# Optimization experiments

Hardware: AMD Instinct MI355X
Metric: run time of the kernel (lower is better)

Reference implementation:

```python
import jax, jax.numpy as jnp
import numpy as np

B, H, S, D = 4, 16, 2048, 64
NEG = -1000000000.0


def setup_inputs() -> dict:
    key = jax.random.key(0)
    kq, kk, kv, km = jax.random.split(key, 4)
    Q = jax.random.normal(kq, (B, H, S, D), dtype=jnp.float32)
    K = jax.random.normal(kk, (B, H, S, D), dtype=jnp.float32)
    V = jax.random.normal(kv, (B, H, S, D), dtype=jnp.float32)
    attn_mask = jax.random.randint(km, (B, 1, 1, S), 0, 2).astype(jnp.bool_)
    return {"Q": Q, "K": K, "V": V, "attn_mask": attn_mask}


def reference(Q, K, V, attn_mask):
    scale = 1.0 / (Q.shape[-1] ** 0.5)
    # [B,H,S,S] scores, masked, softmax over keys
    scores = jnp.einsum("bhqd,bhkd->bhqk", Q, K) * scale
    scores = jnp.where(attn_mask, NEG, scores)
    attn_prob = jax.nn.softmax(scores, axis=-1)
    context = jnp.einsum("bhqk,bhkd->bhqd", attn_prob, V)
    return context
```

## Files before the change

### kernel.cpp

```cpp
#include <hip/hip_runtime.h>
#include <hip/hip_bf16.h>

#define B_ 4
#define H_ 16
#define S_ 2048
#define D_ 64
#define BH_ (B_ * H_)
#define VSTR 2048

#define QS 0.18033688011112042f

typedef __bf16 bf16_t;
typedef __attribute__((ext_vector_type(8))) bf16_t bf16x8;
typedef __attribute__((ext_vector_type(4))) bf16_t bf16x4;
typedef __attribute__((ext_vector_type(4))) float f32x4;

#if __has_builtin(__builtin_amdgcn_exp2f)
#define EX2(x) __builtin_amdgcn_exp2f(x)
#else
#define EX2(x) exp2f(x)
#endif

#define KC_OFF 0u
#define VT_OFF 16777216u
#define CIDX_OFF 33554432u
#define NK_OFF 33619968u

__device__ __forceinline__ bf16x4 cvt4(const float4 a) {
  return (bf16x4){(bf16_t)a.x, (bf16_t)a.y, (bf16_t)a.z, (bf16_t)a.w};
}

__global__ __launch_bounds__(256) void scan_kernel(const unsigned char* __restrict__ raw,
                                                   int* __restrict__ cidx,
                                                   int* __restrict__ nkarr) {
  const int b = blockIdx.x;
  const int tid = threadIdx.x;
  __shared__ int isBool;
  if (tid == 0) isBool = 0;
  __syncthreads();
  int any = 0;
  for (int i = tid; i < B_ * S_; i += 256)
    if ((i & 3) && raw[i]) any = 1;
  if (any) isBool = 1;
  __syncthreads();
  const bool ib = (isBool != 0);

  int flags[8], cnt = 0;
  const int base = tid * 8;
#pragma unroll
  for (int j = 0; j < 8; ++j) {
    const int key = base + j;
    const int m = ib ? (raw[b * S_ + key] ? 1 : 0)
                     : (((const int*)raw)[b * S_ + key] ? 1 : 0);
    flags[j] = m ? 0 : 1;
    cnt += flags[j];
  }
  __shared__ int sc[256];
  sc[tid] = cnt;
  __syncthreads();
  for (int off = 1; off < 256; off <<= 1) {
    const int v = sc[tid];
    const int u = (tid >= off) ? sc[tid - off] : 0;
    __syncthreads();
    sc[tid] = v + u;
    __syncthreads();
  }
  int pos = (tid > 0) ? sc[tid - 1] : 0;
  const int total = sc[255];
  int* cb = cidx + b * VSTR;
#pragma unroll
  for (int j = 0; j < 8; ++j)
    if (flags[j]) cb[pos++] = base + j;
  if (tid == 0) nkarr[b] = total;
  const int padend = ((total + 63) >> 6) << 6;
  for (int i = total + tid; i < padend; i += 256) cb[i] = 0;
}

__global__ __launch_bounds__(256) void gather_kernel(const float* __restrict__ K,
                                                     const float* __restrict__ V,
                                                     const int* __restrict__ cidx,
                                                     const int* __restrict__ nkarr,
                                                     bf16_t* __restrict__ Kc,
                                                     bf16_t* __restrict__ Vtc) {
  const int blk = blockIdx.x;
  const int bh = blk >> 5, tile = blk & 31;
  const int b = bh >> 4;
  if (tile * 64 >= nkarr[b]) return;
  const int tid = threadIdx.x;
  __shared__ int idx[64];
  __shared__ float T[64][65];
  if (tid < 64) idx[tid] = cidx[b * VSTR + tile * 64 + tid];
  __syncthreads();
  {
    const int row = tid >> 2, d0 = (tid & 3) << 4;
    const float* src = K + (size_t)bh * S_ * D_ + (size_t)idx[row] * D_ + d0;
    bf16_t* dst = Kc + (size_t)bh * VSTR * D_ + (size_t)(tile * 64 + row) * D_ + d0;
    const float4 a = ((const float4*)src)[0], bb = ((const float4*)src)[1];
    const float4 c = ((const float4*)src)[2], d = ((const float4*)src)[3];
    *(bf16x4*)(dst) = cvt4(a);
    *(bf16x4*)(dst + 4) = cvt4(bb);
    *(bf16x4*)(dst + 8) = cvt4(c);
    *(bf16x4*)(dst + 12) = cvt4(d);
  }
  const float* vsrc = V + (size_t)bh * S_ * D_;
#pragma unroll
  for (int rep = 0; rep < 4; ++rep) {
    const int i2 = rep * 256 + tid;
    const int row = i2 >> 4, d4 = (i2 & 15) << 2;
    const float4 v = *(const float4*)(vsrc + (size_t)idx[row] * D_ + d4);
    T[row][d4] = v.x; T[row][d4 + 1] = v.y; T[row][d4 + 2] = v.z; T[row][d4 + 3] = v.w;
  }
  __syncthreads();
  bf16_t* vdst = Vtc + (size_t)bh * D_ * VSTR + tile * 64;
#pragma unroll
  for (int rep = 0; rep < 4; ++rep) {
    const int i2 = rep * 256 + tid;
    const int d = i2 >> 4, k4 = (i2 & 15) << 2;
    const bf16x4 o = {(bf16_t)T[k4][d], (bf16_t)T[k4 + 1][d], (bf16_t)T[k4 + 2][d],
                      (bf16_t)T[k4 + 3][d]};
    *(bf16x4*)(vdst + (size_t)d * VSTR + k4) = o;
  }
}


__device__ __forceinline__ bf16x8 pack8(const bf16x4 lo, const bf16x4 hi) {
  bf16x8 r;
  r[0] = lo[0]; r[1] = lo[1]; r[2] = lo[2]; r[3] = lo[3];
  r[4] = hi[0]; r[5] = hi[1]; r[6] = hi[2]; r[7] = hi[3];
  return r;
}

__device__ __forceinline__ bf16x8 qpack(const float4 a, const float4 b) {
  bf16x8 r;
  r[0] = (bf16_t)(a.x * QS); r[1] = (bf16_t)(a.y * QS);
  r[2] = (bf16_t)(a.z * QS); r[3] = (bf16_t)(a.w * QS);
  r[4] = (bf16_t)(b.x * QS); r[5] = (bf16_t)(b.y * QS);
  r[6] = (bf16_t)(b.z * QS); r[7] = (bf16_t)(b.w * QS);
  return r;
}

__global__ __launch_bounds__(512, 4) void attn_main_kernel(const float* __restrict__ Q,
                                                           const bf16_t* __restrict__ Kc,
                                                           const bf16_t* __restrict__ Vtc,
                                                           const int* __restrict__ nkarr,
                                                           float* __restrict__ out) {
  __shared__ bf16_t Kl[2][64][68];
  __shared__ bf16_t Vl[2][64][68];

  const int bid = blockIdx.x;
  const int wu = (bid & 7) * 64 + (bid >> 3);
  const int qt = wu & 7, bh = wu >> 3, b = bh >> 4;

  const int nk = nkarr[b];
  const int nt = (nk + 63) >> 6;

  const int tid = threadIdx.x, wid = tid >> 6, lane = tid & 63;
  const int g4 = ((lane >> 4) & 3) << 2, qi = lane & 15;

  const size_t bhoff = (size_t)bh * (S_ * D_);
  const bf16_t* Kg = Kc + (size_t)bh * VSTR * D_;
  const bf16_t* Vg = Vtc + (size_t)bh * D_ * VSTR;

  const int qrow0 = qt * 256 + wid * 32 + qi;
  bf16x8 qb[2][2];
#pragma unroll
  for (int g = 0; g < 2; ++g) {
    const float* qp = Q + bhoff + (size_t)(qrow0 + g * 16) * D_;
#pragma unroll
    for (int c = 0; c < 2; ++c)
      qb[g][c] = qpack(*(const float4*)(qp + c * 32 + g4),
                       *(const float4*)(qp + c * 32 + 16 + g4));
  }

  const int srow = tid >> 3;
  const int scol = (tid & 7) << 3;

  {
    const uint4 k0 = *(const uint4*)(Kg + (size_t)srow * D_ + scol);
    const uint4 v0 = *(const uint4*)(Vg + (size_t)srow * VSTR + scol);
    *(uint2*)&Kl[0][srow][scol] = make_uint2(k0.x, k0.y);
    *(uint2*)&Kl[0][srow][scol + 4] = make_uint2(k0.z, k0.w);
    *(uint2*)&Vl[0][srow][scol] = make_uint2(v0.x, v0.y);
    *(uint2*)&Vl[0][srow][scol + 4] = make_uint2(v0.z, v0.w);
  }
  __syncthreads();

  f32x4 o[2][4];
#pragma unroll
  for (int g = 0; g < 2; ++g)
#pragma unroll
    for (int dt = 0; dt < 4; ++dt) o[g][dt] = (f32x4){0.f, 0.f, 0.f, 0.f};
  float lrun0 = 0.f, lrun1 = 0.f;

  for (int t = 0; t < nt; ++t) {
    const int cur = t & 1;
    const int nxt = cur ^ 1;
    const bool more = (t + 1 < nt);
    const int kv = (t + 1) * 64;
    const int rem = nk - t * 64;

    uint4 k0, v0;
    if (more) {
      k0 = *(const uint4*)(Kg + (size_t)(kv + srow) * D_ + scol);
      v0 = *(const uint4*)(Vg + (size_t)srow * VSTR + kv + scol);
    }

    bf16x8 pb0[2], pb1[2];
    float ts0 = 0.f, ts1 = 0.f;
    __builtin_amdgcn_s_setprio(1);
#pragma unroll
    for (int kt = 0; kt < 4; ++kt) {
      f32x4 a0 = {0.f, 0.f, 0.f, 0.f}, a1 = a0;
#pragma unroll
      for (int c = 0; c < 2; ++c) {
        const bf16_t* kp = &Kl[cur][kt * 16 + qi][c * 32 + g4];
        const bf16x8 ka = pack8(*(const bf16x4*)kp, *(const bf16x4*)(kp + 16));
        a0 = __builtin_amdgcn_mfma_f32_16x16x32_bf16(ka, qb[0][c], a0, 0, 0, 0);
        a1 = __builtin_amdgcn_mfma_f32_16x16x32_bf16(ka, qb[1][c], a1, 0, 0, 0);
      }
      if (more) {
#pragma unroll
        for (int r = 0; r < 4; ++r) {
          const float p0 = EX2(a0[r]);
          const float p1 = EX2(a1[r]);
          ts0 += p0; ts1 += p1;
          pb0[kt >> 1][(kt & 1) * 4 + r] = (bf16_t)p0;
          pb1[kt >> 1][(kt & 1) * 4 + r] = (bf16_t)p1;
        }
      } else {
#pragma unroll
        for (int r = 0; r < 4; ++r) {
          const int kidx = kt * 16 + g4 + r;
          float p0 = EX2(a0[r]);
          float p1 = EX2(a1[r]);
          p0 = (kidx < rem) ? p0 : 0.f;
          p1 = (kidx < rem) ? p1 : 0.f;
          ts0 += p0; ts1 += p1;
          pb0[kt >> 1][(kt & 1) * 4 + r] = (bf16_t)p0;
          pb1[kt >> 1][(kt & 1) * 4 + r] = (bf16_t)p1;
        }
      }
    }
    __builtin_amdgcn_s_setprio(0);
    lrun0 += ts0;
    lrun1 += ts1;

    if (more) {
      *(uint2*)&Kl[nxt][srow][scol] = make_uint2(k0.x, k0.y);
      *(uint2*)&Kl[nxt][srow][scol + 4] = make_uint2(k0.z, k0.w);
    }

    __builtin_amdgcn_s_setprio(1);
#pragma unroll
    for (int dt = 0; dt < 4; ++dt) {
      const bf16_t* vp0 = &Vl[cur][dt * 16 + qi][g4];
#pragma unroll
      for (int kc = 0; kc < 2; ++kc) {
        const bf16_t* vp = vp0 + kc * 32;
        const bf16x8 va = pack8(*(const bf16x4*)vp, *(const bf16x4*)(vp + 16));
        o[0][dt] = __builtin_amdgcn_mfma_f32_16x16x32_bf16(va, pb0[kc], o[0][dt], 0, 0, 0);
        o[1][dt] = __builtin_amdgcn_mfma_f32_16x16x32_bf16(va, pb1[kc], o[1][dt], 0, 0, 0);
      }
    }
    __builtin_amdgcn_s_setprio(0);

    if (more) {
      *(uint2*)&Vl[nxt][srow][scol] = make_uint2(v0.x, v0.y);
      *(uint2*)&Vl[nxt][srow][scol + 4] = make_uint2(v0.z, v0.w);
      __syncthreads();
    }
  }

#pragma unroll
  for (int g = 0; g < 2; ++g) {
    float lr = g ? lrun1 : lrun0;
    lr += __shfl_xor(lr, 16);
    lr += __shfl_xor(lr, 32);
    const float inv = 1.0f / lr;
    float* op = out + bhoff + (size_t)(qrow0 + g * 16) * D_;
#pragma unroll
    for (int dt = 0; dt < 4; ++dt) {
      float4 w;
      w.x = o[g][dt][0] * inv;
      w.y = o[g][dt][1] * inv;
      w.z = o[g][dt][2] * inv;
      w.w = o[g][dt][3] * inv;
      *(float4*)(op + dt * 16 + g4) = w;
    }
  }
}

extern "C" void kernel_launch(void* const* d_in, const int* in_sizes, int n_in,
                              void* d_out, int out_size, void* d_ws, size_t ws_size,
                              hipStream_t stream) {
  const float* Q = (const float*)d_in[0];
  const float* K = (const float*)d_in[1];
  const float* V = (const float*)d_in[2];
  const unsigned char* mraw = (const unsigned char*)d_in[3];
  float* out = (float*)d_out;

  char* ws = (char*)d_ws;
  bf16_t* Kc = (bf16_t*)(ws + KC_OFF);
  bf16_t* Vtc = (bf16_t*)(ws + VT_OFF);
  int* cidx = (int*)(ws + CIDX_OFF);
  int* nkarr = (int*)(ws + NK_OFF);

  scan_kernel<<<B_, 256, 0, stream>>>(mraw, cidx, nkarr);
  gather_kernel<<<BH_ * 32, 256, 0, stream>>>(K, V, cidx, nkarr, Kc, Vtc);
  attn_main_kernel<<<512, 512, 0, stream>>>(Q, Kc, Vtc, nkarr, out);
}
```

Measured before the change: 70.86 us.

## Prefetch K/V two tiles ahead and compute row sums via MFMA

Global K/V loads are now issued two tiles ahead into alternating register sets, so each load has a full extra iteration to land before it is stored to LDS. Both K and V stores for the next buffer are grouped after the QK phase. The per-lane softmax denominator accumulation and the final cross-lane shuffles are replaced by MFMAs against an all-ones matrix, which take the sum over bf16-rounded probabilities. This moves VALU adds onto the matrix unit but adds four MFMAs per tile and increases register pressure.

```diff
diff --git a/kernel.cpp b/kernel.cpp
--- a/kernel.cpp
+++ b/kernel.cpp
@@ -172,17 +172,28 @@
                        *(const float4*)(qp + c * 32 + 16 + g4));
   }
 
+  bf16x8 ones;
+#pragma unroll
+  for (int j = 0; j < 8; ++j) ones[j] = (bf16_t)1.0f;
+
   const int srow = tid >> 3;
   const int scol = (tid & 7) << 3;
+  const bf16_t* Kgs = Kg + (size_t)srow * D_ + scol;
+  const bf16_t* Vgs = Vg + (size_t)srow * VSTR + scol;
 
   {
-    const uint4 k0 = *(const uint4*)(Kg + (size_t)srow * D_ + scol);
-    const uint4 v0 = *(const uint4*)(Vg + (size_t)srow * VSTR + scol);
+    const uint4 k0 = *(const uint4*)(Kgs);
+    const uint4 v0 = *(const uint4*)(Vgs);
     *(uint2*)&Kl[0][srow][scol] = make_uint2(k0.x, k0.y);
     *(uint2*)&Kl[0][srow][scol + 4] = make_uint2(k0.z, k0.w);
     *(uint2*)&Vl[0][srow][scol] = make_uint2(v0.x, v0.y);
     *(uint2*)&Vl[0][srow][scol + 4] = make_uint2(v0.z, v0.w);
   }
+  uint4 kr0, vr0, kr1, vr1;
+  if (nt > 1) {
+    kr1 = *(const uint4*)(Kgs + (size_t)64 * D_);
+    vr1 = *(const uint4*)(Vgs + 64);
+  }
   __syncthreads();
 
   f32x4 o[2][4];
@@ -190,23 +201,18 @@
   for (int g = 0; g < 2; ++g)
 #pragma unroll
     for (int dt = 0; dt < 4; ++dt) o[g][dt] = (f32x4){0.f, 0.f, 0.f, 0.f};
-  float lrun0 = 0.f, lrun1 = 0.f;
-
-  for (int t = 0; t < nt; ++t) {
-    const int cur = t & 1;
-    const int nxt = cur ^ 1;
-    const bool more = (t + 1 < nt);
-    const int kv = (t + 1) * 64;
+  f32x4 la[2] = {{0.f, 0.f, 0.f, 0.f}, {0.f, 0.f, 0.f, 0.f}};
+
+  auto step = [&](int t, uint4& sk, uint4& sv, uint4& pk, uint4& pv) {
+    const int cur = t & 1, nxt = cur ^ 1;
     const int rem = nk - t * 64;
 
-    uint4 k0, v0;
-    if (more) {
-      k0 = *(const uint4*)(Kg + (size_t)(kv + srow) * D_ + scol);
-      v0 = *(const uint4*)(Vg + (size_t)srow * VSTR + kv + scol);
+    if (t + 2 < nt) {
+      pk = *(const uint4*)(Kgs + (size_t)(t + 2) * 64 * D_);
+      pv = *(const uint4*)(Vgs + (t + 2) * 64);
     }
 
     bf16x8 pb0[2], pb1[2];
-    float ts0 = 0.f, ts1 = 0.f;
     __builtin_amdgcn_s_setprio(1);
 #pragma unroll
     for (int kt = 0; kt < 4; ++kt) {
@@ -218,14 +224,11 @@
         a0 = __builtin_amdgcn_mfma_f32_16x16x32_bf16(ka, qb[0][c], a0, 0, 0, 0);
         a1 = __builtin_amdgcn_mfma_f32_16x16x32_bf16(ka, qb[1][c], a1, 0, 0, 0);
       }
-      if (more) {
+      if (t + 1 < nt) {
 #pragma unroll
         for (int r = 0; r < 4; ++r) {
-          const float p0 = EX2(a0[r]);
-          const float p1 = EX2(a1[r]);
-          ts0 += p0; ts1 += p1;
-          pb0[kt >> 1][(kt & 1) * 4 + r] = (bf16_t)p0;
-          pb1[kt >> 1][(kt & 1) * 4 + r] = (bf16_t)p1;
+          pb0[kt >> 1][(kt & 1) * 4 + r] = (bf16_t)EX2(a0[r]);
+          pb1[kt >> 1][(kt & 1) * 4 + r] = (bf16_t)EX2(a1[r]);
         }
       } else {
 #pragma unroll
@@ -235,22 +238,25 @@
           float p1 = EX2(a1[r]);
           p0 = (kidx < rem) ? p0 : 0.f;
           p1 = (kidx < rem) ? p1 : 0.f;
-          ts0 += p0; ts1 += p1;
           pb0[kt >> 1][(kt & 1) * 4 + r] = (bf16_t)p0;
           pb1[kt >> 1][(kt & 1) * 4 + r] = (bf16_t)p1;
         }
       }
     }
     __builtin_amdgcn_s_setprio(0);
-    lrun0 += ts0;
-    lrun1 += ts1;
-
-    if (more) {
-      *(uint2*)&Kl[nxt][srow][scol] = make_uint2(k0.x, k0.y);
-      *(uint2*)&Kl[nxt][srow][scol + 4] = make_uint2(k0.z, k0.w);
+
+    if (t + 1 < nt) {
+      *(uint2*)&Kl[nxt][srow][scol] = make_uint2(sk.x, sk.y);
+      *(uint2*)&Kl[nxt][srow][scol + 4] = make_uint2(sk.z, sk.w);
+      *(uint2*)&Vl[nxt][srow][scol] = make_uint2(sv.x, sv.y);
+      *(uint2*)&Vl[nxt][srow][scol + 4] = make_uint2(sv.z, sv.w);
     }
 
     __builtin_amdgcn_s_setprio(1);
+    la[0] = __builtin_amdgcn_mfma_f32_16x16x32_bf16(ones, pb0[0], la[0], 0, 0, 0);
+    la[0] = __builtin_amdgcn_mfma_f32_16x16x32_bf16(ones, pb0[1], la[0], 0, 0, 0);
+    la[1] = __builtin_amdgcn_mfma_f32_16x16x32_bf16(ones, pb1[0], la[1], 0, 0, 0);
+    la[1] = __builtin_amdgcn_mfma_f32_16x16x32_bf16(ones, pb1[1], la[1], 0, 0, 0);
 #pragma unroll
     for (int dt = 0; dt < 4; ++dt) {
       const bf16_t* vp0 = &Vl[cur][dt * 16 + qi][g4];
@@ -264,19 +270,17 @@
     }
     __builtin_amdgcn_s_setprio(0);
 
-    if (more) {
-      *(uint2*)&Vl[nxt][srow][scol] = make_uint2(v0.x, v0.y);
-      *(uint2*)&Vl[nxt][srow][scol + 4] = make_uint2(v0.z, v0.w);
-      __syncthreads();
-    }
+    if (t + 1 < nt) __syncthreads();
+  };
+
+  for (int t = 0; t < nt; ++t) {
+    if ((t & 1) == 0) step(t, kr1, vr1, kr0, vr0);
+    else              step(t, kr0, vr0, kr1, vr1);
   }
 
 #pragma unroll
   for (int g = 0; g < 2; ++g) {
-    float lr = g ? lrun1 : lrun0;
-    lr += __shfl_xor(lr, 16);
-    lr += __shfl_xor(lr, 32);
-    const float inv = 1.0f / lr;
+    const float inv = 1.0f / la[g][0];
     float* op = out + bhoff + (size_t)(qrow0 + g * 16) * D_;
 #pragma unroll
     for (int dt = 0; dt < 4; ++dt) {
```

New measurement: 107.0 us. +51.0%, slower.

## Pre-permute K/V in gather and use XOR-swizzled LDS for 128-bit reads

Applied to the files above, without the earlier changes.

The gather kernel now writes K and transposed V in a permuted order so that each MFMA operand's eight bf16 values are contiguous. The main kernel drops the padded 68-wide LDS rows for unpadded rows with an XOR swizzle, storing and loading whole 128-bit vectors instead of pairs of 64-bit pieces. This is meant to halve LDS instruction count and remove the pack8 register shuffling while avoiding bank conflicts. It relies on the permutation and the swizzle matching exactly across both kernels.

```diff
diff --git a/kernel.cpp b/kernel.cpp
--- a/kernel.cpp
+++ b/kernel.cpp
@@ -92,15 +92,16 @@
   if (tid < 64) idx[tid] = cidx[b * VSTR + tile * 64 + tid];
   __syncthreads();
   {
-    const int row = tid >> 2, d0 = (tid & 3) << 4;
-    const float* src = K + (size_t)bh * S_ * D_ + (size_t)idx[row] * D_ + d0;
-    bf16_t* dst = Kc + (size_t)bh * VSTR * D_ + (size_t)(tile * 64 + row) * D_ + d0;
-    const float4 a = ((const float4*)src)[0], bb = ((const float4*)src)[1];
-    const float4 c = ((const float4*)src)[2], d = ((const float4*)src)[3];
-    *(bf16x4*)(dst) = cvt4(a);
-    *(bf16x4*)(dst + 4) = cvt4(bb);
-    *(bf16x4*)(dst + 8) = cvt4(c);
-    *(bf16x4*)(dst + 12) = cvt4(d);
+    const int row = tid >> 2, g = tid & 3;
+    const float* src = K + (size_t)bh * S_ * D_ + (size_t)idx[row] * D_;
+    bf16_t* dst = Kc + (size_t)bh * VSTR * D_ + (size_t)(tile * 64 + row) * D_;
+#pragma unroll
+    for (int c = 0; c < 2; ++c) {
+      const float4 lo = *(const float4*)(src + c * 32 + g * 4);
+      const float4 hi = *(const float4*)(src + c * 32 + 16 + g * 4);
+      *(bf16x4*)(dst + (c * 4 + g) * 8) = cvt4(lo);
+      *(bf16x4*)(dst + (c * 4 + g) * 8 + 4) = cvt4(hi);
+    }
   }
   const float* vsrc = V + (size_t)bh * S_ * D_;
 #pragma unroll
@@ -116,19 +117,15 @@
   for (int rep = 0; rep < 4; ++rep) {
     const int i2 = rep * 256 + tid;
     const int d = i2 >> 4, k4 = (i2 & 15) << 2;
+    const int kc = k4 >> 5, within = k4 & 31;
+    const int g = (within & 15) >> 2, half = (within & 16) ? 4 : 0;
+    const int pos = (kc * 4 + g) * 8 + half;
     const bf16x4 o = {(bf16_t)T[k4][d], (bf16_t)T[k4 + 1][d], (bf16_t)T[k4 + 2][d],
                       (bf16_t)T[k4 + 3][d]};
-    *(bf16x4*)(vdst + (size_t)d * VSTR + k4) = o;
-  }
-}
-
-
-__device__ __forceinline__ bf16x8 pack8(const bf16x4 lo, const bf16x4 hi) {
-  bf16x8 r;
-  r[0] = lo[0]; r[1] = lo[1]; r[2] = lo[2]; r[3] = lo[3];
-  r[4] = hi[0]; r[5] = hi[1]; r[6] = hi[2]; r[7] = hi[3];
-  return r;
-}
+    *(bf16x4*)(vdst + (size_t)d * VSTR + pos) = o;
+  }
+}
+
 
 __device__ __forceinline__ bf16x8 qpack(const float4 a, const float4 b) {
   bf16x8 r;
@@ -144,8 +141,8 @@
                                                            const bf16_t* __restrict__ Vtc,
                                                            const int* __restrict__ nkarr,
                                                            float* __restrict__ out) {
-  __shared__ bf16_t Kl[2][64][68];
-  __shared__ bf16_t Vl[2][64][68];
+  __shared__ bf16_t Kl[2][64][64];
+  __shared__ bf16_t Vl[2][64][64];
 
   const int bid = blockIdx.x;
   const int wu = (bid & 7) * 64 + (bid >> 3);
@@ -155,7 +152,10 @@
   const int nt = (nk + 63) >> 6;
 
   const int tid = threadIdx.x, wid = tid >> 6, lane = tid & 63;
-  const int g4 = ((lane >> 4) & 3) << 2, qi = lane & 15;
+  const int gg = (lane >> 4) & 3, g4 = gg << 2, qi = lane & 15;
+  const int q7 = qi & 7;
+  const int koff0 = ((gg) ^ q7) << 3;
+  const int koff1 = ((4 + gg) ^ q7) << 3;
 
   const size_t bhoff = (size_t)bh * (S_ * D_);
   const bf16_t* Kg = Kc + (size_t)bh * VSTR * D_;
@@ -173,15 +173,16 @@
   }
 
   const int srow = tid >> 3;
-  const int scol = (tid & 7) << 3;
+  const int scc = tid & 7;
+  const int soff = ((scc ^ (srow & 7)) << 3);
+  const bf16_t* Kgs = Kg + (size_t)srow * D_ + scc * 8;
+  const bf16_t* Vgs = Vg + (size_t)srow * VSTR + scc * 8;
 
   {
-    const uint4 k0 = *(const uint4*)(Kg + (size_t)srow * D_ + scol);
-    const uint4 v0 = *(const uint4*)(Vg + (size_t)srow * VSTR + scol);
-    *(uint2*)&Kl[0][srow][scol] = make_uint2(k0.x, k0.y);
-    *(uint2*)&Kl[0][srow][scol + 4] = make_uint2(k0.z, k0.w);
-    *(uint2*)&Vl[0][srow][scol] = make_uint2(v0.x, v0.y);
-    *(uint2*)&Vl[0][srow][scol + 4] = make_uint2(v0.z, v0.w);
+    const uint4 k0 = *(const uint4*)Kgs;
+    const uint4 v0 = *(const uint4*)Vgs;
+    *(uint4*)&Kl[0][srow][soff] = k0;
+    *(uint4*)&Vl[0][srow][soff] = v0;
   }
   __syncthreads();
 
@@ -201,8 +202,8 @@
 
     uint4 k0, v0;
     if (more) {
-      k0 = *(const uint4*)(Kg + (size_t)(kv + srow) * D_ + scol);
-      v0 = *(const uint4*)(Vg + (size_t)srow * VSTR + kv + scol);
+      k0 = *(const uint4*)(Kgs + (size_t)kv * D_);
+      v0 = *(const uint4*)(Vgs + kv);
     }
 
     bf16x8 pb0[2], pb1[2];
@@ -210,13 +211,17 @@
     __builtin_amdgcn_s_setprio(1);
 #pragma unroll
     for (int kt = 0; kt < 4; ++kt) {
+      const bf16_t* krow = &Kl[cur][kt * 16 + qi][0];
       f32x4 a0 = {0.f, 0.f, 0.f, 0.f}, a1 = a0;
-#pragma unroll
-      for (int c = 0; c < 2; ++c) {
-        const bf16_t* kp = &Kl[cur][kt * 16 + qi][c * 32 + g4];
-        const bf16x8 ka = pack8(*(const bf16x4*)kp, *(const bf16x4*)(kp + 16));
-        a0 = __builtin_amdgcn_mfma_f32_16x16x32_bf16(ka, qb[0][c], a0, 0, 0, 0);
-        a1 = __builtin_amdgcn_mfma_f32_16x16x32_bf16(ka, qb[1][c], a1, 0, 0, 0);
+      {
+        const bf16x8 ka = *(const bf16x8*)(krow + koff0);
+        a0 = __builtin_amdgcn_mfma_f32_16x16x32_bf16(ka, qb[0][0], a0, 0, 0, 0);
+        a1 = __builtin_amdgcn_mfma_f32_16x16x32_bf16(ka, qb[1][0], a1, 0, 0, 0);
+      }
+      {
+        const bf16x8 ka = *(const bf16x8*)(krow + koff1);
+        a0 = __builtin_amdgcn_mfma_f32_16x16x32_bf16(ka, qb[0][1], a0, 0, 0, 0);
+        a1 = __builtin_amdgcn_mfma_f32_16x16x32_bf16(ka, qb[1][1], a1, 0, 0, 0);
       }
       if (more) {
 #pragma unroll
@@ -245,28 +250,27 @@
     lrun0 += ts0;
     lrun1 += ts1;
 
+    if (more) *(uint4*)&Kl[nxt][srow][soff] = k0;
+
+    __builtin_amdgcn_s_setprio(1);
+#pragma unroll
+    for (int dt = 0; dt < 4; ++dt) {
+      const bf16_t* vrow = &Vl[cur][dt * 16 + qi][0];
+      {
+        const bf16x8 va = *(const bf16x8*)(vrow + koff0);
+        o[0][dt] = __builtin_amdgcn_mfma_f32_16x16x32_bf16(va, pb0[0], o[0][dt], 0, 0, 0);
+        o[1][dt] = __builtin_amdgcn_mfma_f32_16x16x32_bf16(va, pb1[0], o[1][dt], 0, 0, 0);
+      }
+      {
+        const bf16x8 va = *(const bf16x8*)(vrow + koff1);
+        o[0][dt] = __builtin_amdgcn_mfma_f32_16x16x32_bf16(va, pb0[1], o[0][dt], 0, 0, 0);
+        o[1][dt] = __builtin_amdgcn_mfma_f32_16x16x32_bf16(va, pb1[1], o[1][dt], 0, 0, 0);
+      }
+    }
+    __builtin_amdgcn_s_setprio(0);
+
     if (more) {
-      *(uint2*)&Kl[nxt][srow][scol] = make_uint2(k0.x, k0.y);
-      *(uint2*)&Kl[nxt][srow][scol + 4] = make_uint2(k0.z, k0.w);
-    }
-
-    __builtin_amdgcn_s_setprio(1);
-#pragma unroll
-    for (int dt = 0; dt < 4; ++dt) {
-      const bf16_t* vp0 = &Vl[cur][dt * 16 + qi][g4];
-#pragma unroll
-      for (int kc = 0; kc < 2; ++kc) {
-        const bf16_t* vp = vp0 + kc * 32;
-        const bf16x8 va = pack8(*(const bf16x4*)vp, *(const bf16x4*)(vp + 16));
-        o[0][dt] = __builtin_amdgcn_mfma_f32_16x16x32_bf16(va, pb0[kc], o[0][dt], 0, 0, 0);
-        o[1][dt] = __builtin_amdgcn_mfma_f32_16x16x32_bf16(va, pb1[kc], o[1][dt], 0, 0, 0);
-      }
-    }
-    __builtin_amdgcn_s_setprio(0);
-
-    if (more) {
-      *(uint2*)&Vl[nxt][srow][scol] = make_uint2(v0.x, v0.y);
-      *(uint2*)&Vl[nxt][srow][scol + 4] = make_uint2(v0.z, v0.w);
+      *(uint4*)&Vl[nxt][srow][soff] = v0;
       __syncthreads();
     }
   }
```

After: 71.55 us. No clear change (+1.0%).
